# Performance work log

Hardware: AMD Instinct MI355X
Metric: run time of the kernel (lower is better)

Reference implementation:

```python
import jax, jax.numpy as jnp
import numpy as np

B, C1, C2, C3, N = 32, 64, 16, 16, 8
EPS = 1e-10


def _spd_power(M, p):
    # fractional power of a symmetric PD matrix via eigendecomposition
    w, V = jnp.linalg.eigh(M)
    w = jnp.clip(w, EPS)
    return jnp.einsum('...ik,...k,...jk->...ij', V, w ** p, V)


def setup_inputs() -> dict:
    key = jax.random.key(0)
    G = jax.random.normal(key, (B, C1, C2, C3, N, N), dtype=jnp.float32)
    # well-conditioned SPD matrices: G G^T / n + 0.5 I
    x = jnp.einsum('...ik,...jk->...ij', G, G) / N + 0.5 * jnp.eye(N, dtype=jnp.float32)
    return {"x": x}


def reference(x):
    b, c1, c2, c3, n, _ = x.shape
    seq = c2 * c3
    X = x.reshape(b * c1, seq, n, n)  # (M, seq, n, n)

    # ---- recursiveFM2D: running affine-invariant Frechet mean -------------
    # M_1 = X_1 ; M_k = geodesic(M_{k-1}, X_k, w_k) with w_k = 1/k (k=2..seq)
    weights = 1.0 / jnp.arange(2.0, seq + 1.0, dtype=x.dtype)  # (seq-1,)

    def step(M, inp):
        Xk, wk = inp
        w, V = jnp.linalg.eigh(M)
        sw = jnp.sqrt(jnp.clip(w, EPS))
        Msq = jnp.einsum('...ik,...k,...jk->...ij', V, sw, V)        # M^{1/2}
        Misq = jnp.einsum('...ik,...k,...jk->...ij', V, 1.0 / sw, V)  # M^{-1/2}
        S = Misq @ Xk @ Misq
        S = 0.5 * (S + S.swapaxes(-1, -2))
        Mn = Msq @ _spd_power(S, wk) @ Msq  # M^{1/2} (M^{-1/2} X M^{-1/2})^w M^{1/2}
        return 0.5 * (Mn + Mn.swapaxes(-1, -2)), None

    FM, _ = jax.lax.scan(step, X[:, 0], (X[:, 1:].swapaxes(0, 1), weights))  # (M, n, n)

    # ---- GLmetric: dist(X_i, FM) = trace(log(X^{-1} FM)^2) via SVD ---------
    Y = jnp.broadcast_to(FM[:, None], X.shape)
    inner = jnp.linalg.solve(X, Y)  # X^{-1} @ FM, (M, seq, n, n)
    u, s, vt = jnp.linalg.svd(inner, full_matrices=False)
    L = jnp.einsum('...ik,...k,...kj->...ij', u, jnp.log(jnp.clip(s, EPS)), vt)
    dist = jnp.einsum('...ij,...ji->...', L, L)  # trace(L @ L)
    return dist.reshape(b, c1 * seq)
```

## Files before the change

kernel.cpp:

```cpp
#include <hip/hip_runtime.h>
#include <stdint.h>

#define EPSF    1e-10f
#define NCHAIN  2048
#define SEQ     256
#define NMAT    (NCHAIN*SEQ)

__device__ float g_fm[NCHAIN * 64];

__device__ __forceinline__ float rcpf(float x) { return __builtin_amdgcn_rcpf(x); }
__device__ __forceinline__ float rsqf(float x) { return __builtin_amdgcn_rsqf(x); }
__device__ __forceinline__ float exp2f_(float x) { return __builtin_amdgcn_exp2f(x); }
__device__ __forceinline__ float log2f_(float x) { return __builtin_amdgcn_logf(x); }

__device__ __forceinline__ float bpf(int addr4, float v) {
    return __int_as_float(__builtin_amdgcn_ds_bpermute(addr4, __float_as_int(v)));
}
__device__ __forceinline__ float rlf(float v, int srcLane) {
    return __int_as_float(__builtin_amdgcn_readlane(__float_as_int(v), srcLane));
}
template<int MASK>
__device__ __forceinline__ float sxf(float v) {
    static_assert(MASK > 0 && MASK < 32, "swizzle mask");
    return __int_as_float(__builtin_amdgcn_ds_swizzle(
        __float_as_int(v), (MASK << 10) | 0x1F));
}
template<int CTRL, int RMASK = 0xF, bool BC = true>
__device__ __forceinline__ float dppf(float v) {
    return __int_as_float(__builtin_amdgcn_update_dpp(
        0, __float_as_int(v), CTRL, RMASK, 0xF, BC));
}
template<int M>
__device__ __forceinline__ float cxf(float v) {
    if constexpr      (M == 1) return dppf<0xB1>(v);
    else if constexpr (M == 2) return dppf<0x4E>(v);
    else if constexpr (M == 3) return dppf<0x1B>(v);
    else if constexpr (M == 4) return dppf<0x141>(dppf<0x1B>(v));
    else if constexpr (M == 5) return dppf<0x141>(dppf<0x4E>(v));
    else if constexpr (M == 6) return dppf<0x141>(dppf<0xB1>(v));
    else                       return dppf<0x141>(v);
}
template<int M>
__device__ __forceinline__ float cxd(float v) {
    if constexpr (M == 4 || M == 5 || M == 6) return sxf<M>(v);
    else                                      return cxf<M>(v);
}
template<int M>
__device__ __forceinline__ float rxf(float v, int lane4) {
    if constexpr      (M == 1)       return dppf<0x128>(v);
    else if constexpr ((M << 3) < 32) return sxf<(M << 3)>(v);
    else                              return bpf(lane4 ^ (M << 5), v);
}
template<int M>
__device__ __forceinline__ float dxf(float v, int lane4) {
    if constexpr      (M == 1)       return dppf<0xB1>(dppf<0x128>(v));
    else if constexpr ((M * 9) < 32)  return sxf<(M * 9)>(v);
    else                              return bpf(lane4 ^ (M * 36), v);
}

__device__ __forceinline__ float wave_sum63(float v) {
    v += dppf<0x111>(v);
    v += dppf<0x112>(v);
    v += dppf<0x114>(v);
    v += dppf<0x118>(v);
    v += dppf<0x142, 0xA, false>(v);
    v += dppf<0x143, 0xC, false>(v);
    return v;
}

__device__ __forceinline__ float dot8(const float* __restrict__ a,
                                      const float* __restrict__ b) {
    const float4 a0 = *reinterpret_cast<const float4*>(a);
    const float4 a1 = *reinterpret_cast<const float4*>(a + 4);
    const float4 b0 = *reinterpret_cast<const float4*>(b);
    const float4 b1 = *reinterpret_cast<const float4*>(b + 4);
    float s = a0.x * b0.x;
    s = fmaf(a0.y, b0.y, s); s = fmaf(a0.z, b0.z, s); s = fmaf(a0.w, b0.w, s);
    s = fmaf(a1.x, b1.x, s); s = fmaf(a1.y, b1.y, s); s = fmaf(a1.z, b1.z, s);
    s = fmaf(a1.w, b1.w, s);
    return s;
}

__device__ __forceinline__ void jrot2(float dj, float dm, float apq, float sg,
                                      float &c, float &bs) {
    const float dd = dj - dm;
    const float h  = apq + apq;
    const float r2 = fmaf(dd, dd, fmaf(h, h, 1e-36f));
    const float rr = rsqf(r2);
    const float c2 = fmaf(0.5f * fabsf(dd), rr, 0.5f);
    const float ic = rsqf(c2);
    const float chi = (dd != 0.0f) ? copysignf(1.0f, dd) : sg;
    const bool  tiny = r2 < 1e-33f;
    c  = tiny ? 1.0f : c2 * ic;
    bs = tiny ? 0.0f : apq * chi * rr * ic;
}

template<int M>
__device__ __forceinline__ void jround_fm(float &A, float &W, float &D,
                                          const int lane4, const int j36,
                                          const int tr4, const float sg) {
    const float dmj = cxf<M>(D);
    const float aqj = bpf(j36 ^ (M << 2), A);
    const float Ax  = cxf<M>(A);
    const float Ay  = rxf<M>(A, lane4);
    const float Az  = dxf<M>(A, lane4);
    const float Wc  = cxf<M>(W);
    float aj, bj;
    jrot2(D, dmj, aqj, sg, aj, bj);
    const float ai = bpf(tr4, aj);
    const float bi = bpf(tr4, bj);
    const float t0 = fmaf(bj, Ax, aj * A);
    const float t1 = fmaf(bj, Az, aj * Ay);
    A = fmaf(bi, t1, ai * t0);
    W = fmaf(bj, Wc, aj * W);
    const float d0 = fmaf(bj, aqj, aj * D);
    const float d1 = fmaf(bj, dmj, aj * aqj);
    D = fmaf(bj, d1, aj * d0);
}

template<int M>
__device__ __forceinline__ void jround_d(float &A, float &W, float &D,
                                         const int lane4, const int j36,
                                         const int tr4, const float sg) {
    const float dmj = cxd<M>(D);
    const float aqj = bpf(j36 ^ (M << 2), A);
    float aj, bj;
    jrot2(D, dmj, aqj, sg, aj, bj);
    const float ai = bpf(tr4, aj);
    const float bi = bpf(tr4, bj);
    const float Ac = cxd<M>(A);
    A = fmaf(bj, Ac, aj * A);
    const float Ar = rxf<M>(A, lane4);
    A = fmaf(bi, Ar, ai * A);
    const float Wc = cxd<M>(W);
    W = fmaf(bj, Wc, aj * W);
    const float d0 = fmaf(bj, aqj, aj * D);
    const float d1 = fmaf(bj, dmj, aj * aqj);
    D = fmaf(bj, d1, aj * d0);
}

__global__ void __launch_bounds__(256, 2)
fm_kernel(const float* __restrict__ x) {
    __shared__ __align__(16) float sA[4][64], sB[4][64], sC[4][64];
    const int w = threadIdx.x >> 6;
    float* __restrict__ bufX = sA[w];
    float* __restrict__ bufF = sB[w];
    float* __restrict__ bufW = sC[w];

    const int wid  = (blockIdx.x << 2) + w;
    const int lane = threadIdx.x & 63;
    const int i = lane >> 3, j = lane & 7;
    const int lane4 = lane << 2;
    const int i32_ = i << 5, j4 = j << 2, i4 = i << 2;
    const int i36 = i * 36, j36 = j * 36;
    const int i8f = i << 3, j8f = j << 3;
    const int tr4 = ((j << 3) + i) << 2;

    const float sg1 = (lane & 1) ? 1.0f : -1.0f;
    const float sg2 = (lane & 2) ? 1.0f : -1.0f;
    const float sg4 = (lane & 4) ? 1.0f : -1.0f;

    const float* __restrict__ base = x + (size_t)wid * (SEQ * 64);

    float Mv = base[lane];
    float Ev = (i == j) ? 1.0f : 0.0f;
    #pragma unroll
    for (int kk = 0; kk < 8; ++kk) {
        const float piv = rlf(Mv, kk * 9);
        const float rp  = rcpf(piv);
        const float Mik = bpf(i32_ + (kk << 2), Mv);
        const float Mkj = bpf((kk << 5) + j4,   Mv);
        const float Ekj = bpf((kk << 5) + j4,   Ev);
        const float mi  = (i > kk) ? Mik * rp : 0.0f;
        Mv = fmaf(-mi, Mkj, Mv);
        Ev = fmaf(-mi, Ekj, Ev);
    }
    float Fi = rsqf(bpf(i36, Mv)) * Ev;

    float Xnext = base[(1 << 6) + lane];

    #pragma unroll 1
    for (int k = 1; k < SEQ; ++k) {
        const float Xv = Xnext;
        const int kn = (k + 1 < SEQ) ? (k + 1) : k;
        Xnext = base[(kn << 6) + lane];
        const float wk = rcpf((float)(k + 1));

        bufX[lane] = Xv;
        bufF[lane] = Fi;
        const float Wv = dot8(bufF + i8f, bufX + j8f);
        bufW[lane] = Wv;
        float Bv = dot8(bufW + i8f, bufF + j8f);
        Bv = 0.5f * (Bv + bpf(tr4, Bv));

        float D = bpf(j36, Bv);
        float V = (i == j) ? 1.0f : 0.0f;
        const int nswp = (k < 12) ? 4 : 3;
        #pragma unroll 1
        for (int sw = 0; sw < nswp; ++sw) {
            jround_fm<1>(Bv, V, D, lane4, j36, tr4, sg1);
            jround_fm<2>(Bv, V, D, lane4, j36, tr4, sg2);
            jround_fm<3>(Bv, V, D, lane4, j36, tr4, sg2);
            jround_fm<4>(Bv, V, D, lane4, j36, tr4, sg4);
            jround_fm<5>(Bv, V, D, lane4, j36, tr4, sg4);
            jround_fm<6>(Bv, V, D, lane4, j36, tr4, sg4);
            jround_fm<7>(Bv, V, D, lane4, j36, tr4, sg4);
        }

        const float lamI = fmaxf(bpf(i4, D), EPSF);
        const float si   = exp2f_(-0.5f * wk * log2f_(lamI));
        bufW[j8f + i] = V;
        bufX[j8f + i] = Fi;
        Fi = si * dot8(bufW + i8f, bufX + j8f);
    }

    bufX[j8f + i] = Fi;
    float Gv = dot8(bufX + i8f, bufX + j8f);
    float Mw = (i == j) ? 1.0f : 0.0f;
    #pragma unroll
    for (int kk = 0; kk < 8; ++kk) {
        const float pr  = rcpf(rlf(Gv, kk * 9));
        const float gk  = bpf((kk << 5) + j4, Gv) * pr;
        const float mk  = bpf((kk << 5) + j4, Mw) * pr;
        const float gik = bpf(i32_ + (kk << 2), Gv);
        const bool  isk = (i == kk);
        Gv = isk ? gk : fmaf(-gik, gk, Gv);
        Mw = isk ? mk : fmaf(-gik, mk, Mw);
    }
    g_fm[(wid << 6) + lane] = Mw;
}

__global__ void __launch_bounds__(256, 4)
dist_kernel(const float* __restrict__ x, float* __restrict__ out) {
    __shared__ __align__(16) float sAr[4][64];
    __shared__ __align__(16) float sAc[4][64];
    __shared__ __align__(16) float sVc[4][64];
    __shared__ __align__(16) float sTc[4][64];
    const int w = threadIdx.x >> 6;
    float* __restrict__ aRow = sAr[w];
    float* __restrict__ aCol = sAc[w];
    float* __restrict__ vCol = sVc[w];
    float* __restrict__ tCol = sTc[w];

    const int wid  = (blockIdx.x << 2) + w;
    const int lane = threadIdx.x & 63;
    const int i = lane >> 3, j = lane & 7;
    const int lane4 = lane << 2;
    const int i32_ = i << 5, j4 = j << 2;
    const int j36 = j * 36;
    const int i8f = i << 3, j8f = j << 3;
    const int tr4 = ((j << 3) + i) << 2;
    const int chain = wid >> 8;

    const float sg1 = (lane & 1) ? 1.0f : -1.0f;
    const float sg2 = (lane & 2) ? 1.0f : -1.0f;
    const float sg4 = (lane & 4) ? 1.0f : -1.0f;

    float Xw = x[(size_t)wid * 64 + lane];
    float Yv = g_fm[(chain << 6) + lane];

    #pragma unroll
    for (int k = 0; k < 8; ++k) {
        const float pr  = rcpf(rlf(Xw, k * 9));
        const float xk  = bpf((k << 5) + j4, Xw) * pr;
        const float yk  = bpf((k << 5) + j4, Yv) * pr;
        const float xik = bpf(i32_ + (k << 2), Xw);
        const bool  isk = (i == k);
        Xw = isk ? xk : fmaf(-xik, xk, Xw);
        Yv = isk ? yk : fmaf(-xik, yk, Yv);
    }
    const float Av = Yv;

    aRow[lane] = Av;
    aCol[j8f + i] = Av;

    float Bv = dot8(aCol + i8f, aCol + j8f);

    float V = (i == j) ? 1.0f : 0.0f;
    float D = bpf(j36, Bv);
    #pragma unroll 1
    for (int sw = 0; sw < 4; ++sw) {
        jround_d<1>(Bv, V, D, lane4, j36, tr4, sg1);
        jround_d<2>(Bv, V, D, lane4, j36, tr4, sg2);
        jround_d<3>(Bv, V, D, lane4, j36, tr4, sg2);
        jround_d<4>(Bv, V, D, lane4, j36, tr4, sg4);
        jround_d<5>(Bv, V, D, lane4, j36, tr4, sg4);
        jround_d<6>(Bv, V, D, lane4, j36, tr4, sg4);
        jround_d<7>(Bv, V, D, lane4, j36, tr4, sg4);
    }
    const float sig2 = fmaxf(D, 1e-20f);
    const float g = (0.34657359028f * log2f_(sig2)) * rsqf(sig2);

    vCol[j8f + i] = V;
    const float T1 = dot8(aRow + i8f, vCol + j8f);

    tCol[j8f + i] = T1;
    const float C = dot8(vCol + i8f, tCol + j8f);

    const float P  = g * C;
    const float Pt = bpf(tr4, P);

    const float total = wave_sum63(P * Pt);
    if (lane == 63) out[wid] = total;
}

extern "C" void kernel_launch(void* const* d_in, const int* in_sizes, int n_in,
                              void* d_out, int out_size, void* d_ws, size_t ws_size,
                              hipStream_t stream) {
    const float* x = (const float*)d_in[0];
    float* out = (float*)d_out;
    (void)in_sizes; (void)n_in; (void)d_ws; (void)ws_size; (void)out_size;

    hipLaunchKernelGGL(fm_kernel, dim3(NCHAIN / 4), dim3(256), 0, stream, x);
    hipLaunchKernelGGL(dist_kernel, dim3(NMAT / 4), dim3(256), 0, stream, x, out);
}
```

Before: 1.690 ms.

## Fuse Frechet-mean and distance kernels, overlapping inversions with serial recursion

Merges the two kernels into one block per chain. One wave runs the serial Frechet-mean recursion while the other three waves precompute X inverses into a global scratch buffer. After a block barrier, all four waves compute the distances from the shared mean. This aims to hide the inversion and distance work behind the latency-bound recursion and to remove the second launch. The cost is extra global traffic for the inverse scratch and idle waves during the recursion.

```diff
diff --git a/kernel.cpp b/kernel.cpp
--- a/kernel.cpp
+++ b/kernel.cpp
@@ -6,7 +6,7 @@
 #define SEQ     256
 #define NMAT    (NCHAIN*SEQ)
 
-__device__ float g_fm[NCHAIN * 64];
+__device__ float g_xinv[(size_t)NMAT * 64];
 
 __device__ __forceinline__ float rcpf(float x) { return __builtin_amdgcn_rcpf(x); }
 __device__ __forceinline__ float rsqf(float x) { return __builtin_amdgcn_rsqf(x); }
@@ -139,15 +139,16 @@
     D = fmaf(bj, d1, aj * d0);
 }
 
-__global__ void __launch_bounds__(256, 2)
-fm_kernel(const float* __restrict__ x) {
-    __shared__ __align__(16) float sA[4][64], sB[4][64], sC[4][64];
-    const int w = threadIdx.x >> 6;
-    float* __restrict__ bufX = sA[w];
-    float* __restrict__ bufF = sB[w];
-    float* __restrict__ bufW = sC[w];
-
-    const int wid  = (blockIdx.x << 2) + w;
+__global__ void __launch_bounds__(256, 8)
+fused_kernel(const float* __restrict__ x, float* __restrict__ out) {
+    __shared__ __align__(16) float sF[64];
+    __shared__ __align__(16) float sXr[4][64];
+    __shared__ __align__(16) float sAr[4][64];
+    __shared__ __align__(16) float sAc[4][64];
+    __shared__ __align__(16) float sVc[4][64];
+    __shared__ __align__(16) float sTc[4][64];
+
+    const int wave = threadIdx.x >> 6;
     const int lane = threadIdx.x & 63;
     const int i = lane >> 3, j = lane & 7;
     const int lane4 = lane << 2;
@@ -155,153 +156,152 @@
     const int i36 = i * 36, j36 = j * 36;
     const int i8f = i << 3, j8f = j << 3;
     const int tr4 = ((j << 3) + i) << 2;
+    const int chain = blockIdx.x;
 
     const float sg1 = (lane & 1) ? 1.0f : -1.0f;
     const float sg2 = (lane & 2) ? 1.0f : -1.0f;
     const float sg4 = (lane & 4) ? 1.0f : -1.0f;
 
-    const float* __restrict__ base = x + (size_t)wid * (SEQ * 64);
-
-    float Mv = base[lane];
-    float Ev = (i == j) ? 1.0f : 0.0f;
-    #pragma unroll
-    for (int kk = 0; kk < 8; ++kk) {
-        const float piv = rlf(Mv, kk * 9);
-        const float rp  = rcpf(piv);
-        const float Mik = bpf(i32_ + (kk << 2), Mv);
-        const float Mkj = bpf((kk << 5) + j4,   Mv);
-        const float Ekj = bpf((kk << 5) + j4,   Ev);
-        const float mi  = (i > kk) ? Mik * rp : 0.0f;
-        Mv = fmaf(-mi, Mkj, Mv);
-        Ev = fmaf(-mi, Ekj, Ev);
+    const float* __restrict__ base = x + (size_t)chain * (SEQ * 64);
+
+    if (wave == 0) {
+        float* __restrict__ bufX = sXr[0];
+        float* __restrict__ bufF = sAr[0];
+        float* __restrict__ bufW = sAc[0];
+
+        float Mv = base[lane];
+        float Ev = (i == j) ? 1.0f : 0.0f;
+        #pragma unroll
+        for (int kk = 0; kk < 8; ++kk) {
+            const float piv = rlf(Mv, kk * 9);
+            const float rp  = rcpf(piv);
+            const float Mik = bpf(i32_ + (kk << 2), Mv);
+            const float Mkj = bpf((kk << 5) + j4,   Mv);
+            const float Ekj = bpf((kk << 5) + j4,   Ev);
+            const float mi  = (i > kk) ? Mik * rp : 0.0f;
+            Mv = fmaf(-mi, Mkj, Mv);
+            Ev = fmaf(-mi, Ekj, Ev);
+        }
+        float Fi = rsqf(bpf(i36, Mv)) * Ev;
+
+        float Xnext = base[(1 << 6) + lane];
+
+        #pragma unroll 1
+        for (int k = 1; k < SEQ; ++k) {
+            const float Xv = Xnext;
+            const int kn = (k + 1 < SEQ) ? (k + 1) : k;
+            Xnext = base[(kn << 6) + lane];
+            const float wk = rcpf((float)(k + 1));
+
+            bufX[lane] = Xv;
+            bufF[lane] = Fi;
+            const float Wv = dot8(bufF + i8f, bufX + j8f);
+            bufW[lane] = Wv;
+            float Bv = dot8(bufW + i8f, bufF + j8f);
+            Bv = 0.5f * (Bv + bpf(tr4, Bv));
+
+            float D = bpf(j36, Bv);
+            float V = (i == j) ? 1.0f : 0.0f;
+            const int nswp = (k < 12) ? 4 : 3;
+            #pragma unroll 1
+            for (int sw = 0; sw < nswp; ++sw) {
+                jround_fm<1>(Bv, V, D, lane4, j36, tr4, sg1);
+                jround_fm<2>(Bv, V, D, lane4, j36, tr4, sg2);
+                jround_fm<3>(Bv, V, D, lane4, j36, tr4, sg2);
+                jround_fm<4>(Bv, V, D, lane4, j36, tr4, sg4);
+                jround_fm<5>(Bv, V, D, lane4, j36, tr4, sg4);
+                jround_fm<6>(Bv, V, D, lane4, j36, tr4, sg4);
+                jround_fm<7>(Bv, V, D, lane4, j36, tr4, sg4);
+            }
+
+            const float lamI = fmaxf(bpf(i4, D), EPSF);
+            const float si   = exp2f_(-0.5f * wk * log2f_(lamI));
+            bufW[j8f + i] = V;
+            bufX[j8f + i] = Fi;
+            Fi = si * dot8(bufW + i8f, bufX + j8f);
+        }
+
+        bufX[j8f + i] = Fi;
+        float Gv = dot8(bufX + i8f, bufX + j8f);
+        float Mw = (i == j) ? 1.0f : 0.0f;
+        #pragma unroll
+        for (int kk = 0; kk < 8; ++kk) {
+            const float pr  = rcpf(rlf(Gv, kk * 9));
+            const float gk  = bpf((kk << 5) + j4, Gv) * pr;
+            const float mk  = bpf((kk << 5) + j4, Mw) * pr;
+            const float gik = bpf(i32_ + (kk << 2), Gv);
+            const bool  isk = (i == kk);
+            Gv = isk ? gk : fmaf(-gik, gk, Gv);
+            Mw = isk ? mk : fmaf(-gik, mk, Mw);
+        }
+        sF[lane] = Mw;
+    } else {
+        #pragma unroll 1
+        for (int t = wave - 1; t < SEQ; t += 3) {
+            const size_t gid = (((size_t)chain << 8) + t) * 64;
+            float Xw = x[(size_t)chain * (SEQ * 64) + (t << 6) + lane];
+            float Yv = (i == j) ? 1.0f : 0.0f;
+            #pragma unroll
+            for (int k = 0; k < 8; ++k) {
+                const float pr  = rcpf(rlf(Xw, k * 9));
+                const float xk  = bpf((k << 5) + j4, Xw) * pr;
+                const float yk  = bpf((k << 5) + j4, Yv) * pr;
+                const float xik = bpf(i32_ + (k << 2), Xw);
+                const bool  isk = (i == k);
+                Xw = isk ? xk : fmaf(-xik, xk, Xw);
+                Yv = isk ? yk : fmaf(-xik, yk, Yv);
+            }
+            g_xinv[gid + lane] = Yv;
+        }
     }
-    float Fi = rsqf(bpf(i36, Mv)) * Ev;
-
-    float Xnext = base[(1 << 6) + lane];
-
+
+    __syncthreads();
+
+    float* __restrict__ xinvR = sXr[wave];
+    float* __restrict__ aRow  = sAr[wave];
+    float* __restrict__ aCol  = sAc[wave];
+    float* __restrict__ vCol  = sVc[wave];
+    float* __restrict__ tCol  = sTc[wave];
+
+    float Xi = g_xinv[(((size_t)chain << 8) + wave) * 64 + lane];
     #pragma unroll 1
-    for (int k = 1; k < SEQ; ++k) {
-        const float Xv = Xnext;
-        const int kn = (k + 1 < SEQ) ? (k + 1) : k;
-        Xnext = base[(kn << 6) + lane];
-        const float wk = rcpf((float)(k + 1));
-
-        bufX[lane] = Xv;
-        bufF[lane] = Fi;
-        const float Wv = dot8(bufF + i8f, bufX + j8f);
-        bufW[lane] = Wv;
-        float Bv = dot8(bufW + i8f, bufF + j8f);
-        Bv = 0.5f * (Bv + bpf(tr4, Bv));
-
+    for (int t = wave; t < SEQ; t += 4) {
+        const float XiCur = Xi;
+        const int tn = (t + 4 < SEQ) ? (t + 4) : t;
+        Xi = g_xinv[(((size_t)chain << 8) + tn) * 64 + lane];
+
+        xinvR[lane] = XiCur;
+        const float Av = dot8(xinvR + i8f, sF + j8f);
+        aRow[lane] = Av;
+        aCol[j8f + i] = Av;
+
+        float Bv = dot8(aCol + i8f, aCol + j8f);
+
+        float V = (i == j) ? 1.0f : 0.0f;
         float D = bpf(j36, Bv);
-        float V = (i == j) ? 1.0f : 0.0f;
-        const int nswp = (k < 12) ? 4 : 3;
         #pragma unroll 1
-        for (int sw = 0; sw < nswp; ++sw) {
-            jround_fm<1>(Bv, V, D, lane4, j36, tr4, sg1);
-            jround_fm<2>(Bv, V, D, lane4, j36, tr4, sg2);
-            jround_fm<3>(Bv, V, D, lane4, j36, tr4, sg2);
-            jround_fm<4>(Bv, V, D, lane4, j36, tr4, sg4);
-            jround_fm<5>(Bv, V, D, lane4, j36, tr4, sg4);
-            jround_fm<6>(Bv, V, D, lane4, j36, tr4, sg4);
-            jround_fm<7>(Bv, V, D, lane4, j36, tr4, sg4);
-        }
-
-        const float lamI = fmaxf(bpf(i4, D), EPSF);
-        const float si   = exp2f_(-0.5f * wk * log2f_(lamI));
-        bufW[j8f + i] = V;
-        bufX[j8f + i] = Fi;
-        Fi = si * dot8(bufW + i8f, bufX + j8f);
+        for (int sw = 0; sw < 4; ++sw) {
+            jround_d<1>(Bv, V, D, lane4, j36, tr4, sg1);
+            jround_d<2>(Bv, V, D, lane4, j36, tr4, sg2);
+            jround_d<3>(Bv, V, D, lane4, j36, tr4, sg2);
+            jround_d<4>(Bv, V, D, lane4, j36, tr4, sg4);
+            jround_d<5>(Bv, V, D, lane4, j36, tr4, sg4);
+            jround_d<6>(Bv, V, D, lane4, j36, tr4, sg4);
+            jround_d<7>(Bv, V, D, lane4, j36, tr4, sg4);
+        }
+        const float sig2 = fmaxf(D, 1e-20f);
+        const float g = (0.34657359028f * log2f_(sig2)) * rsqf(sig2);
+
+        vCol[j8f + i] = V;
+        const float T1 = dot8(aRow + i8f, vCol + j8f);
+        tCol[j8f + i] = T1;
+        const float C = dot8(vCol + i8f, tCol + j8f);
+
+        const float P  = g * C;
+        const float Pt = bpf(tr4, P);
+        const float total = wave_sum63(P * Pt);
+        if (lane == 63) out[(chain << 8) + t] = total;
     }
-
-    bufX[j8f + i] = Fi;
-    float Gv = dot8(bufX + i8f, bufX + j8f);
-    float Mw = (i == j) ? 1.0f : 0.0f;
-    #pragma unroll
-    for (int kk = 0; kk < 8; ++kk) {
-        const float pr  = rcpf(rlf(Gv, kk * 9));
-        const float gk  = bpf((kk << 5) + j4, Gv) * pr;
-        const float mk  = bpf((kk << 5) + j4, Mw) * pr;
-        const float gik = bpf(i32_ + (kk << 2), Gv);
-        const bool  isk = (i == kk);
-        Gv = isk ? gk : fmaf(-gik, gk, Gv);
-        Mw = isk ? mk : fmaf(-gik, mk, Mw);
-    }
-    g_fm[(wid << 6) + lane] = Mw;
-}
-
-__global__ void __launch_bounds__(256, 4)
-dist_kernel(const float* __restrict__ x, float* __restrict__ out) {
-    __shared__ __align__(16) float sAr[4][64];
-    __shared__ __align__(16) float sAc[4][64];
-    __shared__ __align__(16) float sVc[4][64];
-    __shared__ __align__(16) float sTc[4][64];
-    const int w = threadIdx.x >> 6;
-    float* __restrict__ aRow = sAr[w];
-    float* __restrict__ aCol = sAc[w];
-    float* __restrict__ vCol = sVc[w];
-    float* __restrict__ tCol = sTc[w];
-
-    const int wid  = (blockIdx.x << 2) + w;
-    const int lane = threadIdx.x & 63;
-    const int i = lane >> 3, j = lane & 7;
-    const int lane4 = lane << 2;
-    const int i32_ = i << 5, j4 = j << 2;
-    const int j36 = j * 36;
-    const int i8f = i << 3, j8f = j << 3;
-    const int tr4 = ((j << 3) + i) << 2;
-    const int chain = wid >> 8;
-
-    const float sg1 = (lane & 1) ? 1.0f : -1.0f;
-    const float sg2 = (lane & 2) ? 1.0f : -1.0f;
-    const float sg4 = (lane & 4) ? 1.0f : -1.0f;
-
-    float Xw = x[(size_t)wid * 64 + lane];
-    float Yv = g_fm[(chain << 6) + lane];
-
-    #pragma unroll
-    for (int k = 0; k < 8; ++k) {
-        const float pr  = rcpf(rlf(Xw, k * 9));
-        const float xk  = bpf((k << 5) + j4, Xw) * pr;
-        const float yk  = bpf((k << 5) + j4, Yv) * pr;
-        const float xik = bpf(i32_ + (k << 2), Xw);
-        const bool  isk = (i == k);
-        Xw = isk ? xk : fmaf(-xik, xk, Xw);
-        Yv = isk ? yk : fmaf(-xik, yk, Yv);
-    }
-    const float Av = Yv;
-
-    aRow[lane] = Av;
-    aCol[j8f + i] = Av;
-
-    float Bv = dot8(aCol + i8f, aCol + j8f);
-
-    float V = (i == j) ? 1.0f : 0.0f;
-    float D = bpf(j36, Bv);
-    #pragma unroll 1
-    for (int sw = 0; sw < 4; ++sw) {
-        jround_d<1>(Bv, V, D, lane4, j36, tr4, sg1);
-        jround_d<2>(Bv, V, D, lane4, j36, tr4, sg2);
-        jround_d<3>(Bv, V, D, lane4, j36, tr4, sg2);
-        jround_d<4>(Bv, V, D, lane4, j36, tr4, sg4);
-        jround_d<5>(Bv, V, D, lane4, j36, tr4, sg4);
-        jround_d<6>(Bv, V, D, lane4, j36, tr4, sg4);
-        jround_d<7>(Bv, V, D, lane4, j36, tr4, sg4);
-    }
-    const float sig2 = fmaxf(D, 1e-20f);
-    const float g = (0.34657359028f * log2f_(sig2)) * rsqf(sig2);
-
-    vCol[j8f + i] = V;
-    const float T1 = dot8(aRow + i8f, vCol + j8f);
-
-    tCol[j8f + i] = T1;
-    const float C = dot8(vCol + i8f, tCol + j8f);
-
-    const float P  = g * C;
-    const float Pt = bpf(tr4, P);
-
-    const float total = wave_sum63(P * Pt);
-    if (lane == 63) out[wid] = total;
 }
 
 extern "C" void kernel_launch(void* const* d_in, const int* in_sizes, int n_in,
@@ -311,6 +311,5 @@
     float* out = (float*)d_out;
     (void)in_sizes; (void)n_in; (void)d_ws; (void)ws_size; (void)out_size;
 
-    hipLaunchKernelGGL(fm_kernel, dim3(NCHAIN / 4), dim3(256), 0, stream, x);
-    hipLaunchKernelGGL(dist_kernel, dim3(NMAT / 4), dim3(256), 0, stream, x, out);
-}
+    hipLaunchKernelGGL(fused_kernel, dim3(NCHAIN), dim3(256), 0, stream, x, out);
+}
```

Result: slower. 1.751 ms (+3.6%).
